# Kernel tuning notes

Measured on AMD Instinct MI355X. Metric: run time of the kernel, lower is better.

The kernel has to match this reference:

```python
import jax, jax.numpy as jnp
import numpy as np
import math

K = 3          # wavelet order
ALPHA = 5      # fourier modes
LLEV = 0       # coarsest level
CVAL = 1       # channel multiplicity
K2 = K * K     # 9
B, NX, NY, T = 8, 64, 64, 64


def _linear(x, w, b):
    # torch nn.Linear: y = x @ W^T + b, W is [out, in]
    return jnp.einsum('...i,oi->...o', x, w) + b


def _wavelet_transform(x, ec_d, ec_s):
    # strided 4-way gather + concat along channel, then small matmuls
    xa = jnp.concatenate([x[:, ::2, ::2], x[:, ::2, 1::2],
                          x[:, 1::2, ::2], x[:, 1::2, 1::2]], axis=-1)
    return jnp.matmul(xa, ec_d), jnp.matmul(xa, ec_s)


def _even_odd(x, rc_ee, rc_eo, rc_oe, rc_oo):
    b, nx, ny, t, c, ich = x.shape
    k2 = ich // 2
    x_ee = jnp.matmul(x, rc_ee)
    x_eo = jnp.matmul(x, rc_eo)
    x_oe = jnp.matmul(x, rc_oe)
    x_oo = jnp.matmul(x, rc_oo)
    # interleave along Ny then Nx (equivalent to strided scatter into zeros)
    e = jnp.stack([x_ee, x_eo], axis=3).reshape(b, nx, 2 * ny, t, c, k2)
    o = jnp.stack([x_oe, x_oo], axis=3).reshape(b, nx, 2 * ny, t, c, k2)
    return jnp.stack([e, o], axis=2).reshape(b, 2 * nx, 2 * ny, t, c, k2)


def _kernel_ft(x, w1, w2, w3, w4, lo_w, lo_b):
    # sparseKernelFT3d
    b, nx, ny, t, c, ich = x.shape
    xr = x.reshape(b, nx, ny, t, c * ich).transpose(0, 4, 1, 2, 3)  # [B,C,Nx,Ny,T]
    xf = jnp.fft.rfftn(xr, axes=(-3, -2, -1))
    m = ALPHA
    l1 = min(m, nx // 2 + 1)
    l2 = min(m, ny // 2 + 1)
    cm = lambda a, w: jnp.einsum('bixyz,ioxyz->boxyz', a, w)
    w1c = w1[..., 0] + 1j * w1[..., 1]
    w2c = w2[..., 0] + 1j * w2[..., 1]
    w3c = w3[..., 0] + 1j * w3[..., 1]
    w4c = w4[..., 0] + 1j * w4[..., 1]
    out = jnp.zeros((b, c * ich, nx, ny, t // 2 + 1), dtype=xf.dtype)
    out = out.at[:, :, :l1, :l2, :m].set(cm(xf[:, :, :l1, :l2, :m], w1c[:, :, :l1, :l2, :]))
    out = out.at[:, :, nx - l1:, :l2, :m].set(cm(xf[:, :, nx - l1:, :l2, :m], w2c[:, :, :l1, :l2, :]))
    out = out.at[:, :, :l1, ny - l2:, :m].set(cm(xf[:, :, :l1, ny - l2:, :m], w3c[:, :, :l1, :l2, :]))
    out = out.at[:, :, nx - l1:, ny - l2:, :m].set(cm(xf[:, :, nx - l1:, ny - l2:, :m], w4c[:, :, :l1, :l2, :]))
    y = jnp.fft.irfftn(out, s=(nx, ny, t), axes=(-3, -2, -1))
    y = jax.nn.relu(y.transpose(0, 2, 3, 4, 1))
    y = _linear(y, lo_w, lo_b)
    return y.reshape(b, nx, ny, t, c, ich)


def _kernel_conv(x, cw, cb, lw, lb):
    # sparseKernel3d: conv3d(3,1,1) + ReLU, then Linear
    b, nx, ny, t, c, ich = x.shape
    xr = x.reshape(b, nx, ny, t, c * ich).transpose(0, 4, 1, 2, 3)
    y = jax.lax.conv_general_dilated(xr, cw, (1, 1, 1), 'SAME',
                                     dimension_numbers=('NCDHW', 'OIDHW', 'NCDHW'))
    y = jax.nn.relu(y + cb[None, :, None, None, None])
    y = _linear(y.transpose(0, 2, 3, 4, 1), lw, lb)
    return y.reshape(b, nx, ny, t, c, ich)


def setup_inputs() -> dict:
    key = jax.random.key(0)
    ks = jax.random.split(key, 24)
    r = lambda i, shp, s: jax.random.normal(ks[i], shp, dtype=jnp.float32) * s
    return {
        'x': r(0, (B, NX, NY, T, CVAL, K2), 1.0),
        'ec_s': r(1, (4 * K2, K2), 0.2), 'ec_d': r(2, (4 * K2, K2), 0.2),
        'rc_ee': r(3, (2 * K2, K2), 0.25), 'rc_eo': r(4, (2 * K2, K2), 0.25),
        'rc_oe': r(5, (2 * K2, K2), 0.25), 'rc_oo': r(6, (2 * K2, K2), 0.25),
        'w1': r(7, (K2, K2, ALPHA, ALPHA, ALPHA, 2), 0.05),
        'w2': r(8, (K2, K2, ALPHA, ALPHA, ALPHA, 2), 0.05),
        'w3': r(9, (K2, K2, ALPHA, ALPHA, ALPHA, 2), 0.05),
        'w4': r(10, (K2, K2, ALPHA, ALPHA, ALPHA, 2), 0.05),
        'A_Lo_w': r(11, (K2, K2), 0.2), 'A_Lo_b': r(12, (K2,), 0.1),
        'B_conv_w': r(13, (K2, K2, 3, 3, 3), 0.06), 'B_conv_b': r(14, (K2,), 0.1),
        'B_Lo_w': r(15, (K2, K2), 0.2), 'B_Lo_b': r(16, (K2,), 0.1),
        'C_conv_w': r(17, (K2, K2, 3, 3, 3), 0.06), 'C_conv_b': r(18, (K2,), 0.1),
        'C_Lo_w': r(19, (K2, K2), 0.2), 'C_Lo_b': r(20, (K2,), 0.1),
        'T0_w': r(21, (K2, K2), 0.2), 'T0_b': r(22, (K2,), 0.1),
    }


def reference(x, ec_s, ec_d, rc_ee, rc_eo, rc_oe, rc_oo, w1, w2, w3, w4,
              A_Lo_w, A_Lo_b, B_conv_w, B_conv_b, B_Lo_w, B_Lo_b,
              C_conv_w, C_conv_b, C_Lo_w, C_Lo_b, T0_w, T0_b):
    b, nx, ny, t, c, ich = x.shape
    ns = int(math.floor(math.log2(nx)))
    Ud, Us = [], []
    for _ in range(ns - LLEV):  # decompose
        d, x = _wavelet_transform(x, ec_d, ec_s)
        Ud.append(_kernel_ft(d, w1, w2, w3, w4, A_Lo_w, A_Lo_b)
                  + _kernel_conv(x, B_conv_w, B_conv_b, B_Lo_w, B_Lo_b))
        Us.append(_kernel_conv(d, C_conv_w, C_conv_b, C_Lo_w, C_Lo_b))
    n0 = 2 ** LLEV
    x = _linear(x.reshape(b, n0, n0, t, c * ich), T0_w, T0_b)
    x = x.reshape(b, n0, n0, t, c, ich)
    for i in range(ns - 1 - LLEV, -1, -1):  # reconstruct
        x = x + Us[i]
        x = jnp.concatenate([x, Ud[i]], axis=-1)
        x = _even_odd(x, rc_ee, rc_eo, rc_oe, rc_oo)
    return x
```

## Files before the change

### kernel.cpp

```cpp
#include <hip/hip_runtime.h>

#define TWO_PI 6.283185307179586f

struct Meta {
    int bz[7], by[7], bxm[7], bix[7], biz[7], bcv[7];
    int n[6], l1[6], L[6], NT[6];
    int soff[6];
    int tAo[6], tBo[6], tDo[6];
};

__device__ __forceinline__ int find_lev(const int* pre) {
    int lev = 0;
    #pragma unroll
    for (int i = 1; i < 6; ++i) lev += (int)(blockIdx.x >= (unsigned)pre[i]);
    return lev;
}

__global__ void wavelet_kernel(const float* __restrict__ x,
                               float* __restrict__ d, float* __restrict__ s,
                               const float* __restrict__ ec_d,
                               const float* __restrict__ ec_s,
                               int n, int total)
{
    __shared__ float wd[324], wsm[324];
    for (int i = threadIdx.x; i < 324; i += blockDim.x) { wd[i] = ec_d[i]; wsm[i] = ec_s[i]; }
    __syncthreads();
    int idx = blockIdx.x * blockDim.x + threadIdx.x;
    if (idx >= total) return;
    int it = idx & 63; int tmp = idx >> 6;
    int iy = tmp % n; tmp /= n;
    int ix = tmp % n; int b = tmp / n;
    int n2 = 2 * n;
    const float* base = x + ((((size_t)(b * n2 + 2 * ix) * n2 + 2 * iy) * 64 + it) * 9);
    const float* p0 = base;
    const float* p1 = base + 64 * 9;
    const float* p2 = base + (size_t)n2 * 64 * 9;
    const float* p3 = p2 + 64 * 9;
    float a[36];
    #pragma unroll
    for (int k = 0; k < 9; ++k) { a[k] = p0[k]; a[9+k] = p1[k]; a[18+k] = p2[k]; a[27+k] = p3[k]; }
    size_t ob = (size_t)idx * 9;
    #pragma unroll
    for (int oc = 0; oc < 9; ++oc) {
        float vd = 0.f, vs = 0.f;
        #pragma unroll
        for (int k = 0; k < 36; ++k) { vd += a[k] * wd[k*9+oc]; vs += a[k] * wsm[k*9+oc]; }
        d[ob+oc] = vd; s[ob+oc] = vs;
    }
}

__global__ __launch_bounds__(256, 2)
void conv2_kernel(const float* __restrict__ s_all, float* __restrict__ ud_all,
                  const float* __restrict__ d_all, float* __restrict__ us_all,
                  const float* __restrict__ Bcw, const float* __restrict__ Bcb,
                  const float* __restrict__ Blw, const float* __restrict__ Blb,
                  const float* __restrict__ Ccw, const float* __restrict__ Ccb,
                  const float* __restrict__ Clw, const float* __restrict__ Clb,
                  Meta m)
{
    const int which = blockIdx.y;
    const float* cw = which ? Ccw : Bcw;
    const float* cb = which ? Ccb : Bcb;
    const float* lw = which ? Clw : Blw;
    const float* lb = which ? Clb : Blb;

    __shared__ float scw2[2430];
    __shared__ float slw[81], scb[9], slb[9];
    for (int i = threadIdx.x; i < 2187; i += 256) {
        int wo = i / 81, rem = i % 81, o = rem / 9, ic = rem % 9;
        scw2[(wo * 9 + o) * 10 + ic] = cw[(o * 9 + ic) * 27 + wo];
    }
    if (threadIdx.x < 81) slw[threadIdx.x] = lw[threadIdx.x];
    if (threadIdx.x < 9) { scb[threadIdx.x] = cb[threadIdx.x]; slb[threadIdx.x] = lb[threadIdx.x]; }
    __syncthreads();

    int lev = find_lev(m.bcv);
    int n = m.n[lev];
    int idx = (blockIdx.x - m.bcv[lev]) * 256 + threadIdx.x;
    int nh = (n + 1) >> 1;
    int total = 8 * n * nh * 64;
    if (idx >= total) return;
    int t = idx & 63; int tmp = idx >> 6;
    int iy0 = (tmp % nh) * 2; tmp /= nh;
    int ix = tmp % n; int b = tmp / n;
    bool has1 = (iy0 + 1) < n;
    const float* in = (which ? d_all : s_all) + (size_t)m.soff[lev] * 576;
    float* out      = (which ? us_all : ud_all) + (size_t)m.soff[lev] * 576;

    float acc0[9], acc1[9];
    #pragma unroll
    for (int o = 0; o < 9; ++o) { acc0[o] = scb[o]; acc1[o] = scb[o]; }

    for (int dd = 0; dd < 9; ++dd) {
        int dx = dd / 3 - 1, dt = dd % 3 - 1;
        int jx = ix + dx, jt = t + dt;
        bool okxt = ((unsigned)jx < (unsigned)n) && ((unsigned)jt < 64u);
        const float* rowbase = in + (((size_t)(b * n + (okxt ? jx : 0)) * n) * 64
                                     + (okxt ? jt : 0)) * 9;
        float va[9], vb[9];
        {
            int jy = iy0 - 1; bool ok = okxt && (jy >= 0);
            const float* p = rowbase + (size_t)(ok ? jy : 0) * 576;
            #pragma unroll
            for (int ic = 0; ic < 9; ++ic) va[ic] = ok ? p[ic] : 0.f;
            const float* q = rowbase + (size_t)iy0 * 576;
            #pragma unroll
            for (int ic = 0; ic < 9; ++ic) vb[ic] = okxt ? q[ic] : 0.f;
        }
        #pragma unroll
        for (int k = 0; k < 3; ++k) {
            const float* wbase = &scw2[(((dx + 1) * 3 + k) * 3 + (dt + 1)) * 90];
            #pragma unroll
            for (int o = 0; o < 9; ++o) {
                const float* wp = wbase + o * 10;
                float2 w01 = *(const float2*)(wp);
                float2 w23 = *(const float2*)(wp + 2);
                float2 w45 = *(const float2*)(wp + 4);
                float2 w67 = *(const float2*)(wp + 6);
                float  w8  = wp[8];
                acc0[o] += va[0]*w01.x + va[1]*w01.y + va[2]*w23.x + va[3]*w23.y
                         + va[4]*w45.x + va[5]*w45.y + va[6]*w67.x + va[7]*w67.y + va[8]*w8;
                acc1[o] += vb[0]*w01.x + vb[1]*w01.y + vb[2]*w23.x + vb[3]*w23.y
                         + vb[4]*w45.x + vb[5]*w45.y + vb[6]*w67.x + vb[7]*w67.y + vb[8]*w8;
            }
            if (k < 2) {
                int jy = iy0 + k + 1; bool ok = okxt && (jy < n);
                const float* p = rowbase + (size_t)(ok ? jy : 0) * 576;
                #pragma unroll
                for (int ic = 0; ic < 9; ++ic) { va[ic] = vb[ic]; vb[ic] = ok ? p[ic] : 0.f; }
            }
        }
    }
    {
        float r[9];
        #pragma unroll
        for (int o = 0; o < 9; ++o) r[o] = fmaxf(acc0[o], 0.f);
        size_t ob = (((size_t)(b * n + ix) * n + iy0) * 64 + t) * 9;
        #pragma unroll
        for (int o2 = 0; o2 < 9; ++o2) {
            float vv = slb[o2];
            #pragma unroll
            for (int o = 0; o < 9; ++o) vv += r[o] * slw[o2 * 9 + o];
            if (which == 0) out[ob + o2] += vv; else out[ob + o2] = vv;
        }
    }
    if (has1) {
        float r[9];
        #pragma unroll
        for (int o = 0; o < 9; ++o) r[o] = fmaxf(acc1[o], 0.f);
        size_t ob = (((size_t)(b * n + ix) * n + iy0 + 1) * 64 + t) * 9;
        #pragma unroll
        for (int o2 = 0; o2 < 9; ++o2) {
            float vv = slb[o2];
            #pragma unroll
            for (int o = 0; o < 9; ++o) vv += r[o] * slw[o2 * 9 + o];
            if (which == 0) out[ob + o2] += vv; else out[ob + o2] = vv;
        }
    }
}

__global__ void fwdz_kernel(const float* __restrict__ d_all, float2* __restrict__ tA, Meta m)
{
    int lev = find_lev(m.bz);
    int n = m.n[lev];
    int idx = (blockIdx.x - m.bz[lev]) * 256 + threadIdx.x;
    int total = 8 * n * n * 45;
    if (idx >= total) return;
    int ic = idx % 9; int tmp = idx / 9;
    int kz = tmp % 5; int site = tmp / 5;
    const float* p = d_all + (size_t)(m.soff[lev] + site) * 576 + ic;
    float re = 0.f, im = 0.f;
    for (int it = 0; it < 64; ++it) {
        int mm = (kz * it) & 63;
        float sv, cv; __sincosf((TWO_PI / 64.0f) * mm, &sv, &cv);
        float v = p[(size_t)it * 9];
        re += v * cv; im -= v * sv;
    }
    tA[m.tAo[lev] + idx] = make_float2(re, im);
}

__global__ void fwdy_kernel(const float2* __restrict__ tA, float2* __restrict__ tB, Meta m)
{
    int lev = find_lev(m.by);
    int n = m.n[lev], l1 = m.l1[lev], L = m.L[lev];
    int idx = (blockIdx.x - m.by[lev]) * 256 + threadIdx.x;
    int total = 8 * n * L * 45;
    if (idx >= total) return;
    int c45 = idx % 45; int tmp = idx / 45;
    int kyI = tmp % L; tmp /= L;
    int ix = tmp % n; int b = tmp / n;
    int ky = (kyI < l1) ? kyI : (n - L + kyI);
    const float2* p = tA + m.tAo[lev] + ((size_t)(b * n + ix) * n) * 45 + c45;
    float re = 0.f, im = 0.f;
    for (int iy = 0; iy < n; ++iy) {
        int mm = (ky * iy) & (n - 1);
        float sv, cv; __sincosf((TWO_PI / n) * mm, &sv, &cv);
        float2 a = p[(size_t)iy * 45];
        re += a.x * cv + a.y * sv;
        im += a.y * cv - a.x * sv;
    }
    tB[m.tBo[lev] + idx] = make_float2(re, im);
}

__global__ void fwdxmix_kernel(const float2* __restrict__ tB, float2* __restrict__ tD,
                               const float* __restrict__ w1, const float* __restrict__ w2,
                               const float* __restrict__ w3, const float* __restrict__ w4,
                               Meta m)
{
    __shared__ float2 sFzy[32 * 45];
    __shared__ float2 sF[10 * 45];
    int lev = find_lev(m.bxm);
    int n = m.n[lev], l1 = m.l1[lev], L = m.L[lev];
    int lb = blockIdx.x - m.bxm[lev];
    int kyI = lb % L;
    int b   = lb / L;
    int ky = (kyI < l1) ? kyI : (n - L + kyI);
    int nload = n * 45;
    for (int i = threadIdx.x; i < nload; i += blockDim.x) {
        int ix = i / 45, c = i % 45;
        sFzy[i] = tB[m.tBo[lev] + ((size_t)(b * n + ix) * L + kyI) * 45 + c];
    }
    __syncthreads();
    int nf = L * 45;
    for (int i = threadIdx.x; i < nf; i += blockDim.x) {
        int kxI = i / 45, c = i % 45;
        int kx = (kxI < l1) ? kxI : (n - L + kxI);
        float re = 0.f, im = 0.f;
        for (int ix = 0; ix < n; ++ix) {
            int mm = (kx * ix) & (n - 1);
            float sv, cv; __sincosf((TWO_PI / n) * mm, &sv, &cv);
            float2 a = sFzy[ix * 45 + c];
            re += a.x * cv + a.y * sv;
            im += a.y * cv - a.x * sv;
        }
        sF[i] = make_float2(re, im);
    }
    __syncthreads();
    bool ly = ky < l1, hy = ky >= n - l1;
    for (int i = threadIdx.x; i < nf; i += blockDim.x) {
        int kxI = i / 45, c = i % 45;
        int kz = c / 9, oc = c % 9;
        int kx = (kxI < l1) ? kxI : (n - L + kxI);
        bool lx = kx < l1, hx = kx >= n - l1;
        const float* w; int wx, wy;
        if (hx && hy)      { w = w4; wx = kx - (n - l1); wy = ky - (n - l1); }
        else if (lx && hy) { w = w3; wx = kx;            wy = ky - (n - l1); }
        else if (hx && ly) { w = w2; wx = kx - (n - l1); wy = ky; }
        else               { w = w1; wx = kx;            wy = ky; }
        const float* wb = w + (((size_t)oc * 5 + wx) * 5 + wy) * 10 + kz * 2;
        const float2* pf = &sF[kxI * 45 + kz * 9];
        float re = 0.f, im = 0.f;
        #pragma unroll
        for (int ic = 0; ic < 9; ++ic) {
            float2 a = pf[ic];
            float wr = wb[(size_t)ic * 2250];
            float wi = wb[(size_t)ic * 2250 + 1];
            re += a.x * wr - a.y * wi;
            im += a.x * wi + a.y * wr;
        }
        tD[m.tDo[lev] + (((size_t)(b * L + kxI) * L + kyI) * 5 + kz) * 9 + oc] = make_float2(re, im);
    }
}

__global__ void invx_kernel(const float2* __restrict__ tD, float2* __restrict__ tB, Meta m)
{
    int lev = find_lev(m.bix);
    int n = m.n[lev], l1 = m.l1[lev], L = m.L[lev];
    int idx = (blockIdx.x - m.bix[lev]) * 256 + threadIdx.x;
    int total = 8 * n * L * 45;
    if (idx >= total) return;
    int c45 = idx % 45; int tmp = idx / 45;
    int kyI = tmp % L; tmp /= L;
    int ix = tmp % n; int b = tmp / n;
    const float2* p = tD + m.tDo[lev] + ((size_t)b * L * L) * 45 + (size_t)kyI * 45 + c45;
    float re = 0.f, im = 0.f;
    for (int kxI = 0; kxI < L; ++kxI) {
        int kx = (kxI < l1) ? kxI : (n - L + kxI);
        int mm = (kx * ix) & (n - 1);
        float sv, cv; __sincosf((TWO_PI / n) * mm, &sv, &cv);
        float2 a = p[(size_t)kxI * L * 45];
        re += a.x * cv - a.y * sv;
        im += a.x * sv + a.y * cv;
    }
    tB[m.tBo[lev] + idx] = make_float2(re, im);
}

__global__ void invyz_kernel(const float2* __restrict__ tB, float* __restrict__ ud_all,
                             const float* __restrict__ lw, const float* __restrict__ lb,
                             Meta m)
{
    __shared__ float2 sG1[10 * 45];
    __shared__ float2 sG2[4 * 45];
    __shared__ float slw[81], slb[9];
    int lev = find_lev(m.biz);
    int n = m.n[lev], l1 = m.l1[lev], L = m.L[lev], NT = m.NT[lev];
    int TY = n / NT;
    int lb2 = blockIdx.x - m.biz[lev];
    int iyt = lb2 % NT;
    int ix  = (lb2 / NT) % n;
    int b   = lb2 / (NT * n);
    int iy0 = iyt * TY;
    if (threadIdx.x < 81) slw[threadIdx.x] = lw[threadIdx.x];
    if (threadIdx.x < 9)  slb[threadIdx.x] = lb[threadIdx.x];
    int nload = L * 45;
    for (int i = threadIdx.x; i < nload; i += blockDim.x)
        sG1[i] = tB[m.tBo[lev] + ((size_t)(b * n + ix) * L) * 45 + i];
    __syncthreads();
    int nf = TY * 45;
    for (int i = threadIdx.x; i < nf; i += blockDim.x) {
        int il = i / 45, c = i % 45;
        int iy = iy0 + il;
        float re = 0.f, im = 0.f;
        for (int kyI = 0; kyI < L; ++kyI) {
            int ky = (kyI < l1) ? kyI : (n - L + kyI);
            int mm = (ky * iy) & (n - 1);
            float sv, cv; __sincosf((TWO_PI / n) * mm, &sv, &cv);
            float2 a = sG1[kyI * 45 + c];
            re += a.x * cv - a.y * sv;
            im += a.x * sv + a.y * cv;
        }
        sG2[i] = make_float2(re, im);
    }
    __syncthreads();
    int t = threadIdx.x;
    if (t < TY * 64) {
        int il = t >> 6, it = t & 63;
        float inv_norm = 1.0f / ((float)n * (float)n * 64.0f);
        float cvz[5], svz[5];
        #pragma unroll
        for (int kz = 0; kz < 5; ++kz) {
            int mm = (kz * it) & 63;
            __sincosf((TWO_PI / 64.0f) * mm, &svz[kz], &cvz[kz]);
        }
        const float2* pg = &sG2[il * 45];
        float y[9];
        #pragma unroll
        for (int oc = 0; oc < 9; ++oc) {
            float v = 0.f;
            #pragma unroll
            for (int kz = 0; kz < 5; ++kz) {
                float2 a = pg[kz * 9 + oc];
                float term = a.x * cvz[kz] - a.y * svz[kz];
                v += (kz == 0 ? 1.0f : 2.0f) * term;
            }
            y[oc] = fmaxf(v * inv_norm, 0.f);
        }
        size_t ob = ((size_t)(m.soff[lev] + (b * n + ix) * n + iy0 + il) * 64 + it) * 9;
        #pragma unroll
        for (int o2 = 0; o2 < 9; ++o2) {
            float v = slb[o2];
            #pragma unroll
            for (int oc = 0; oc < 9; ++oc) v += y[oc] * slw[o2 * 9 + oc];
            ud_all[ob + o2] = v;
        }
    }
}

__global__ void recon_kernel(const float* __restrict__ x, const float* __restrict__ Us,
                             const float* __restrict__ Ud, float* __restrict__ out,
                             const float* __restrict__ ree, const float* __restrict__ reo,
                             const float* __restrict__ roe, const float* __restrict__ roo,
                             const float* __restrict__ t0w, const float* __restrict__ t0b,
                             int n, int total, int apply_t0)
{
    __shared__ float s_m[4][162];
    __shared__ float st0[81], st0b[9];
    for (int i = threadIdx.x; i < 162; i += blockDim.x) {
        s_m[0][i] = ree[i]; s_m[1][i] = reo[i]; s_m[2][i] = roe[i]; s_m[3][i] = roo[i];
    }
    if (threadIdx.x < 81) st0[threadIdx.x] = t0w[threadIdx.x];
    if (threadIdx.x < 9)  st0b[threadIdx.x] = t0b[threadIdx.x];
    __syncthreads();
    int idx = blockIdx.x * blockDim.x + threadIdx.x;
    if (idx >= total) return;
    int it = idx & 63; int tmp = idx >> 6;
    int iy = tmp % n; tmp /= n;
    int ix = tmp % n; int b = tmp / n;
    float v[18];
    size_t ib = (size_t)idx * 9;
    if (apply_t0) {
        float xr[9];
        #pragma unroll
        for (int k = 0; k < 9; ++k) xr[k] = x[ib+k];
        #pragma unroll
        for (int o = 0; o < 9; ++o) {
            float r = st0b[o];
            #pragma unroll
            for (int i = 0; i < 9; ++i) r += xr[i] * st0[o*9+i];
            v[o] = r + Us[ib+o];
        }
    } else {
        #pragma unroll
        for (int k = 0; k < 9; ++k) v[k] = x[ib+k] + Us[ib+k];
    }
    #pragma unroll
    for (int k = 0; k < 9; ++k) v[9+k] = Ud[ib+k];
    int n2 = 2 * n;
    #pragma unroll
    for (int q = 0; q < 4; ++q) {
        int rx = q >> 1, ry = q & 1;
        size_t ob = ((((size_t)(b * n2 + 2*ix + rx) * n2) + 2*iy + ry) * 64 + it) * 9;
        const float* mm = s_m[q];
        #pragma unroll
        for (int oc = 0; oc < 9; ++oc) {
            float r = 0.f;
            #pragma unroll
            for (int k = 0; k < 18; ++k) r += v[k] * mm[k*9+oc];
            out[ob + oc] = r;
        }
    }
}

extern "C" void kernel_launch(void* const* d_in, const int* in_sizes, int n_in,
                              void* d_out, int out_size, void* d_ws, size_t ws_size,
                              hipStream_t stream)
{
    const float* x0    = (const float*)d_in[0];
    const float* ec_s  = (const float*)d_in[1];
    const float* ec_d  = (const float*)d_in[2];
    const float* rc_ee = (const float*)d_in[3];
    const float* rc_eo = (const float*)d_in[4];
    const float* rc_oe = (const float*)d_in[5];
    const float* rc_oo = (const float*)d_in[6];
    const float* w1    = (const float*)d_in[7];
    const float* w2    = (const float*)d_in[8];
    const float* w3    = (const float*)d_in[9];
    const float* w4    = (const float*)d_in[10];
    const float* A_Lo_w = (const float*)d_in[11];
    const float* A_Lo_b = (const float*)d_in[12];
    const float* B_cw  = (const float*)d_in[13];
    const float* B_cb  = (const float*)d_in[14];
    const float* B_lw  = (const float*)d_in[15];
    const float* B_lb  = (const float*)d_in[16];
    const float* C_cw  = (const float*)d_in[17];
    const float* C_cb  = (const float*)d_in[18];
    const float* C_lw  = (const float*)d_in[19];
    const float* C_lb  = (const float*)d_in[20];
    const float* T0_w  = (const float*)d_in[21];
    const float* T0_b  = (const float*)d_in[22];

    Meta m;
    int ns_[6] = {32, 16, 8, 4, 2, 1};
    int az = 0, ay = 0, axm = 0, aix = 0, aiz = 0, acv = 0;
    int aS = 0, aA = 0, aB = 0, aD = 0;
    for (int l = 0; l < 6; ++l) {
        int n = ns_[l];
        int l1 = (n / 2 + 1 < 5) ? (n / 2 + 1) : 5;
        int L = (2 * l1 < n) ? 2 * l1 : n;
        int TY = (n < 4) ? n : 4;
        int NT = n / TY;
        int nh = (n + 1) / 2;
        m.n[l] = n; m.l1[l] = l1; m.L[l] = L; m.NT[l] = NT;
        m.soff[l] = aS; m.tAo[l] = aA; m.tBo[l] = aB; m.tDo[l] = aD;
        m.bz[l] = az; m.by[l] = ay; m.bxm[l] = axm; m.bix[l] = aix; m.biz[l] = aiz; m.bcv[l] = acv;
        az  += (8 * n * n * 45 + 255) / 256;
        ay  += (8 * n * L * 45 + 255) / 256;
        axm += 8 * L;
        aix += (8 * n * L * 45 + 255) / 256;
        aiz += 8 * n * NT;
        acv += (8 * n * nh * 64 + 255) / 256;
        aS += 8 * n * n; aA += 8 * n * n * 45; aB += 8 * n * L * 45; aD += 8 * L * L * 45;
    }
    m.bz[6] = az; m.by[6] = ay; m.bxm[6] = axm; m.bix[6] = aix; m.biz[6] = aiz; m.bcv[6] = acv;

    float* ws = (float*)d_ws;
    size_t off = 0;
    auto alloc = [&](size_t nf) { float* p = ws + off; off += (nf + 3) & ~(size_t)3; return p; };
    size_t NSf = (size_t)aS * 576;
    float* d_all  = alloc(NSf);
    float* s_all  = alloc(NSf);
    float* ud_all = alloc(NSf);
    float* us_all = alloc(NSf);
    float2* tA = (float2*)alloc((size_t)aA * 2);
    float2* tB = (float2*)alloc((size_t)aB * 2);
    float2* tD = (float2*)alloc((size_t)aD * 2);
    float* pingA = alloc((size_t)8 * 32 * 32 * 64 * 9);
    float* pingB = alloc((size_t)8 * 16 * 16 * 64 * 9);

    const int BLK = 256;

    for (int lev = 0; lev < 6; ++lev) {
        int n = ns_[lev];
        const float* xin = (lev == 0) ? x0 : (s_all + (size_t)m.soff[lev-1] * 576);
        int total = 8 * n * n * 64;
        wavelet_kernel<<<(total + BLK - 1) / BLK, BLK, 0, stream>>>(
            xin, d_all + (size_t)m.soff[lev] * 576, s_all + (size_t)m.soff[lev] * 576,
            ec_d, ec_s, n, total);
    }

    fwdz_kernel  <<<az,  BLK, 0, stream>>>(d_all, tA, m);
    fwdy_kernel  <<<ay,  BLK, 0, stream>>>(tA, tB, m);
    fwdxmix_kernel<<<axm, BLK, 0, stream>>>(tB, tD, w1, w2, w3, w4, m);
    invx_kernel  <<<aix, BLK, 0, stream>>>(tD, tB, m);
    invyz_kernel <<<aiz, BLK, 0, stream>>>(tB, ud_all, A_Lo_w, A_Lo_b, m);
    dim3 cgrid(acv, 2);
    conv2_kernel <<<cgrid, BLK, 0, stream>>>(s_all, ud_all, d_all, us_all,
                                             B_cw, B_cb, B_lw, B_lb,
                                             C_cw, C_cb, C_lw, C_lb, m);

    float* cur = nullptr;
    for (int lev = 5; lev >= 0; --lev) {
        int n = ns_[lev];
        int total = 8 * n * n * 64;
        const float* xin = (lev == 5) ? (s_all + (size_t)m.soff[5] * 576) : cur;
        float* outp = (lev == 0) ? (float*)d_out : ((lev & 1) ? pingA : pingB);
        recon_kernel<<<(total + BLK - 1) / BLK, BLK, 0, stream>>>(
            xin, us_all + (size_t)m.soff[lev] * 576, ud_all + (size_t)m.soff[lev] * 576, outp,
            rc_ee, rc_eo, rc_oe, rc_oo, T0_w, T0_b, n, total, (lev == 5) ? 1 : 0);
        cur = outp;
    }
}
```

Before: 577.4 us.

## Switch intermediate buffers from interleaved channels to channel-major per site

Stores every intermediate per-site tensor as [channel][time] rather than [time][channel], so that neighbouring threads (adjacent time steps) touch consecutive addresses in the wavelet, conv, forward-z FFT, inverse output and reconstruction kernels. Only the first wavelet input and the final reconstruction output keep the original interleaved layout. The aim is fully coalesced loads and stores in place of stride-9 access, and the cost is extra branching on layout flags plus a layout change every kernel must agree on.

```diff
diff --git a/kernel.cpp b/kernel.cpp
--- a/kernel.cpp
+++ b/kernel.cpp
@@ -16,11 +16,12 @@
     return lev;
 }
 
+
 __global__ void wavelet_kernel(const float* __restrict__ x,
                                float* __restrict__ d, float* __restrict__ s,
                                const float* __restrict__ ec_d,
                                const float* __restrict__ ec_s,
-                               int n, int total)
+                               int n, int total, int aos_in)
 {
     __shared__ float wd[324], wsm[324];
     for (int i = threadIdx.x; i < 324; i += blockDim.x) { wd[i] = ec_d[i]; wsm[i] = ec_s[i]; }
@@ -31,21 +32,31 @@
     int iy = tmp % n; tmp /= n;
     int ix = tmp % n; int b = tmp / n;
     int n2 = 2 * n;
-    const float* base = x + ((((size_t)(b * n2 + 2 * ix) * n2 + 2 * iy) * 64 + it) * 9);
-    const float* p0 = base;
-    const float* p1 = base + 64 * 9;
-    const float* p2 = base + (size_t)n2 * 64 * 9;
-    const float* p3 = p2 + 64 * 9;
     float a[36];
-    #pragma unroll
-    for (int k = 0; k < 9; ++k) { a[k] = p0[k]; a[9+k] = p1[k]; a[18+k] = p2[k]; a[27+k] = p3[k]; }
-    size_t ob = (size_t)idx * 9;
+    if (aos_in) {
+        const float* base = x + ((((size_t)(b * n2 + 2 * ix) * n2 + 2 * iy) * 64 + it) * 9);
+        const float* p0 = base;
+        const float* p1 = base + 576;
+        const float* p2 = base + (size_t)n2 * 576;
+        const float* p3 = p2 + 576;
+        #pragma unroll
+        for (int k = 0; k < 9; ++k) { a[k] = p0[k]; a[9+k] = p1[k]; a[18+k] = p2[k]; a[27+k] = p3[k]; }
+    } else {
+        const float* base = x + ((size_t)(b * n2 + 2 * ix) * n2 + 2 * iy) * 576 + it;
+        const float* p0 = base;
+        const float* p1 = base + 576;
+        const float* p2 = base + (size_t)n2 * 576;
+        const float* p3 = p2 + 576;
+        #pragma unroll
+        for (int k = 0; k < 9; ++k) { a[k] = p0[k*64]; a[9+k] = p1[k*64]; a[18+k] = p2[k*64]; a[27+k] = p3[k*64]; }
+    }
+    size_t ob = (size_t)(idx >> 6) * 576 + it;
     #pragma unroll
     for (int oc = 0; oc < 9; ++oc) {
         float vd = 0.f, vs = 0.f;
         #pragma unroll
         for (int k = 0; k < 36; ++k) { vd += a[k] * wd[k*9+oc]; vs += a[k] * wsm[k*9+oc]; }
-        d[ob+oc] = vd; s[ob+oc] = vs;
+        d[ob + oc*64] = vd; s[ob + oc*64] = vs;
     }
 }
 
@@ -95,17 +106,17 @@
         int dx = dd / 3 - 1, dt = dd % 3 - 1;
         int jx = ix + dx, jt = t + dt;
         bool okxt = ((unsigned)jx < (unsigned)n) && ((unsigned)jt < 64u);
-        const float* rowbase = in + (((size_t)(b * n + (okxt ? jx : 0)) * n) * 64
-                                     + (okxt ? jt : 0)) * 9;
+        const float* rowbase = in + ((size_t)(b * n + (okxt ? jx : 0)) * n) * 576
+                                  + (okxt ? jt : 0);
         float va[9], vb[9];
         {
             int jy = iy0 - 1; bool ok = okxt && (jy >= 0);
             const float* p = rowbase + (size_t)(ok ? jy : 0) * 576;
             #pragma unroll
-            for (int ic = 0; ic < 9; ++ic) va[ic] = ok ? p[ic] : 0.f;
+            for (int ic = 0; ic < 9; ++ic) va[ic] = ok ? p[ic*64] : 0.f;
             const float* q = rowbase + (size_t)iy0 * 576;
             #pragma unroll
-            for (int ic = 0; ic < 9; ++ic) vb[ic] = okxt ? q[ic] : 0.f;
+            for (int ic = 0; ic < 9; ++ic) vb[ic] = okxt ? q[ic*64] : 0.f;
         }
         #pragma unroll
         for (int k = 0; k < 3; ++k) {
@@ -127,7 +138,7 @@
                 int jy = iy0 + k + 1; bool ok = okxt && (jy < n);
                 const float* p = rowbase + (size_t)(ok ? jy : 0) * 576;
                 #pragma unroll
-                for (int ic = 0; ic < 9; ++ic) { va[ic] = vb[ic]; vb[ic] = ok ? p[ic] : 0.f; }
+                for (int ic = 0; ic < 9; ++ic) { va[ic] = vb[ic]; vb[ic] = ok ? p[ic*64] : 0.f; }
             }
         }
     }
@@ -135,26 +146,26 @@
         float r[9];
         #pragma unroll
         for (int o = 0; o < 9; ++o) r[o] = fmaxf(acc0[o], 0.f);
-        size_t ob = (((size_t)(b * n + ix) * n + iy0) * 64 + t) * 9;
+        size_t ob = (size_t)((b * n + ix) * n + iy0) * 576 + t;
         #pragma unroll
         for (int o2 = 0; o2 < 9; ++o2) {
             float vv = slb[o2];
             #pragma unroll
             for (int o = 0; o < 9; ++o) vv += r[o] * slw[o2 * 9 + o];
-            if (which == 0) out[ob + o2] += vv; else out[ob + o2] = vv;
+            if (which == 0) out[ob + o2*64] += vv; else out[ob + o2*64] = vv;
         }
     }
     if (has1) {
         float r[9];
         #pragma unroll
         for (int o = 0; o < 9; ++o) r[o] = fmaxf(acc1[o], 0.f);
-        size_t ob = (((size_t)(b * n + ix) * n + iy0 + 1) * 64 + t) * 9;
+        size_t ob = (size_t)((b * n + ix) * n + iy0 + 1) * 576 + t;
         #pragma unroll
         for (int o2 = 0; o2 < 9; ++o2) {
             float vv = slb[o2];
             #pragma unroll
             for (int o = 0; o < 9; ++o) vv += r[o] * slw[o2 * 9 + o];
-            if (which == 0) out[ob + o2] += vv; else out[ob + o2] = vv;
+            if (which == 0) out[ob + o2*64] += vv; else out[ob + o2*64] = vv;
         }
     }
 }
@@ -168,12 +179,12 @@
     if (idx >= total) return;
     int ic = idx % 9; int tmp = idx / 9;
     int kz = tmp % 5; int site = tmp / 5;
-    const float* p = d_all + (size_t)(m.soff[lev] + site) * 576 + ic;
+    const float* p = d_all + (size_t)(m.soff[lev] + site) * 576 + ic * 64;
     float re = 0.f, im = 0.f;
     for (int it = 0; it < 64; ++it) {
         int mm = (kz * it) & 63;
         float sv, cv; __sincosf((TWO_PI / 64.0f) * mm, &sv, &cv);
-        float v = p[(size_t)it * 9];
+        float v = p[it];
         re += v * cv; im -= v * sv;
     }
     tA[m.tAo[lev] + idx] = make_float2(re, im);
@@ -345,13 +356,13 @@
             }
             y[oc] = fmaxf(v * inv_norm, 0.f);
         }
-        size_t ob = ((size_t)(m.soff[lev] + (b * n + ix) * n + iy0 + il) * 64 + it) * 9;
+        size_t ob = (size_t)(m.soff[lev] + (b * n + ix) * n + iy0 + il) * 576 + it;
         #pragma unroll
         for (int o2 = 0; o2 < 9; ++o2) {
             float v = slb[o2];
             #pragma unroll
             for (int oc = 0; oc < 9; ++oc) v += y[oc] * slw[o2 * 9 + oc];
-            ud_all[ob + o2] = v;
+            ud_all[ob + o2*64] = v;
         }
     }
 }
@@ -361,7 +372,7 @@
                              const float* __restrict__ ree, const float* __restrict__ reo,
                              const float* __restrict__ roe, const float* __restrict__ roo,
                              const float* __restrict__ t0w, const float* __restrict__ t0b,
-                             int n, int total, int apply_t0)
+                             int n, int total, int apply_t0, int aos_out)
 {
     __shared__ float s_m[4][162];
     __shared__ float st0[81], st0b[9];
@@ -377,36 +388,48 @@
     int iy = tmp % n; tmp /= n;
     int ix = tmp % n; int b = tmp / n;
     float v[18];
-    size_t ib = (size_t)idx * 9;
+    size_t ib = (size_t)(idx >> 6) * 576 + it;
     if (apply_t0) {
         float xr[9];
         #pragma unroll
-        for (int k = 0; k < 9; ++k) xr[k] = x[ib+k];
+        for (int k = 0; k < 9; ++k) xr[k] = x[ib + k*64];
         #pragma unroll
         for (int o = 0; o < 9; ++o) {
             float r = st0b[o];
             #pragma unroll
             for (int i = 0; i < 9; ++i) r += xr[i] * st0[o*9+i];
-            v[o] = r + Us[ib+o];
+            v[o] = r + Us[ib + o*64];
         }
     } else {
         #pragma unroll
-        for (int k = 0; k < 9; ++k) v[k] = x[ib+k] + Us[ib+k];
+        for (int k = 0; k < 9; ++k) v[k] = x[ib + k*64] + Us[ib + k*64];
     }
     #pragma unroll
-    for (int k = 0; k < 9; ++k) v[9+k] = Ud[ib+k];
+    for (int k = 0; k < 9; ++k) v[9+k] = Ud[ib + k*64];
     int n2 = 2 * n;
     #pragma unroll
     for (int q = 0; q < 4; ++q) {
         int rx = q >> 1, ry = q & 1;
-        size_t ob = ((((size_t)(b * n2 + 2*ix + rx) * n2) + 2*iy + ry) * 64 + it) * 9;
+        size_t site2 = ((size_t)(b * n2 + 2*ix + rx) * n2) + 2*iy + ry;
         const float* mm = s_m[q];
-        #pragma unroll
-        for (int oc = 0; oc < 9; ++oc) {
-            float r = 0.f;
-            #pragma unroll
-            for (int k = 0; k < 18; ++k) r += v[k] * mm[k*9+oc];
-            out[ob + oc] = r;
+        if (aos_out) {
+            size_t ob = (site2 * 64 + it) * 9;
+            #pragma unroll
+            for (int oc = 0; oc < 9; ++oc) {
+                float r = 0.f;
+                #pragma unroll
+                for (int k = 0; k < 18; ++k) r += v[k] * mm[k*9+oc];
+                out[ob + oc] = r;
+            }
+        } else {
+            size_t ob = site2 * 576 + it;
+            #pragma unroll
+            for (int oc = 0; oc < 9; ++oc) {
+                float r = 0.f;
+                #pragma unroll
+                for (int k = 0; k < 18; ++k) r += v[k] * mm[k*9+oc];
+                out[ob + oc*64] = r;
+            }
         }
     }
 }
@@ -485,7 +508,7 @@
         int total = 8 * n * n * 64;
         wavelet_kernel<<<(total + BLK - 1) / BLK, BLK, 0, stream>>>(
             xin, d_all + (size_t)m.soff[lev] * 576, s_all + (size_t)m.soff[lev] * 576,
-            ec_d, ec_s, n, total);
+            ec_d, ec_s, n, total, (lev == 0) ? 1 : 0);
     }
 
     fwdz_kernel  <<<az,  BLK, 0, stream>>>(d_all, tA, m);
@@ -506,7 +529,8 @@
         float* outp = (lev == 0) ? (float*)d_out : ((lev & 1) ? pingA : pingB);
         recon_kernel<<<(total + BLK - 1) / BLK, BLK, 0, stream>>>(
             xin, us_all + (size_t)m.soff[lev] * 576, ud_all + (size_t)m.soff[lev] * 576, outp,
-            rc_ee, rc_eo, rc_oe, rc_oo, T0_w, T0_b, n, total, (lev == 5) ? 1 : 0);
+            rc_ee, rc_eo, rc_oe, rc_oo, T0_w, T0_b, n, total,
+            (lev == 5) ? 1 : 0, (lev == 0) ? 1 : 0);
         cur = outp;
     }
 }
```

After: 651.2 us. +12.8%, slower.
